# Kernel optimization log

Hardware: AMD Instinct MI355X
Metric: run time of the kernel (lower is better)

Reference implementation:

```python
import jax, jax.numpy as jnp
import numpy as np

DIM = 768
HID = 3072
E_SPEC = 4
E_SHARED = 2
TOP_K = 2
LN_EPS = 1e-5


def _expert_stack_params(key, n_experts):
    k1, k2, k3, k4 = jax.random.split(key, 4)
    s1 = 1.0 / np.sqrt(DIM)
    s2 = 1.0 / np.sqrt(HID)
    return {
        'w1': jax.random.uniform(k1, (n_experts, DIM, HID), minval=-s1, maxval=s1, dtype=jnp.float32),
        'b1': jax.random.uniform(k2, (n_experts, HID), minval=-s1, maxval=s1, dtype=jnp.float32),
        'w2': jax.random.uniform(k3, (n_experts, HID, DIM), minval=-s2, maxval=s2, dtype=jnp.float32),
        'b2': jax.random.uniform(k4, (n_experts, DIM), minval=-s2, maxval=s2, dtype=jnp.float32),
    }


def setup_inputs() -> dict:
    key = jax.random.key(0)
    ks = jax.random.split(key, 8)
    B, N = 64, 196
    s = 1.0 / np.sqrt(DIM)
    spec = _expert_stack_params(ks[1], E_SPEC)
    shared = _expert_stack_params(ks[2], E_SHARED)
    return {
        'x': jax.random.normal(ks[0], (B, N, DIM), dtype=jnp.float32),
        'ln_gamma': jnp.ones((DIM,), jnp.float32),
        'ln_beta': jnp.zeros((DIM,), jnp.float32),
        'spec_router_w': jax.random.uniform(ks[3], (DIM, E_SPEC), minval=-s, maxval=s, dtype=jnp.float32),
        'spec_router_b': jnp.zeros((E_SPEC,), jnp.float32),
        'spec_w1': spec['w1'], 'spec_b1': spec['b1'], 'spec_w2': spec['w2'], 'spec_b2': spec['b2'],
        'shared_router_w': jax.random.uniform(ks[4], (DIM, E_SHARED), minval=-s, maxval=s, dtype=jnp.float32),
        'shared_router_b': jnp.zeros((E_SHARED,), jnp.float32),
        'sh_w1': shared['w1'], 'sh_b1': shared['b1'], 'sh_w2': shared['w2'], 'sh_b2': shared['b2'],
    }


def _all_experts(x, w1, b1, w2, b2):
    # x: [B,N,D]; w1: [E,D,H] -> out: [B,N,E,D]
    h = jnp.einsum('bnd,edh->bneh', x, w1) + b1
    h = jax.nn.gelu(h, approximate=False)  # torch nn.GELU default is exact
    return jnp.einsum('bneh,ehd->bned', h, w2) + b2


def reference(x, ln_gamma, ln_beta,
              spec_router_w, spec_router_b, spec_w1, spec_b1, spec_w2, spec_b2,
              shared_router_w, shared_router_b, sh_w1, sh_b1, sh_w2, sh_b2):
    # LayerNorm
    mu = jnp.mean(x, axis=-1, keepdims=True)
    var = jnp.mean(jnp.square(x - mu), axis=-1, keepdims=True)
    xn = (x - mu) * jax.lax.rsqrt(var + LN_EPS) * ln_gamma + ln_beta

    # Specific-expert branch: dense all-expert compute, then top-k gather (faithful)
    spec_logits = xn @ spec_router_w + spec_router_b            # [B,N,E]
    spec_probs = jax.nn.softmax(spec_logits, axis=-1)
    topk_probs, topk_idx = jax.lax.top_k(spec_probs, TOP_K)    # [B,N,K]
    spec_out_all = _all_experts(xn, spec_w1, spec_b1, spec_w2, spec_b2)  # [B,N,E,D]
    sel = jnp.take_along_axis(spec_out_all, topk_idx[..., None], axis=2)  # [B,N,K,D]
    specific_out = jnp.sum(topk_probs[..., None] * sel, axis=2)

    # Shared-expert branch: softmax-weighted sum over all experts
    sh_logits = xn @ shared_router_w + shared_router_b          # [B,N,Es]
    sh_probs = jax.nn.softmax(sh_logits, axis=-1)
    sh_out_all = _all_experts(xn, sh_w1, sh_b1, sh_w2, sh_b2)   # [B,N,Es,D]
    shared_out = jnp.einsum('bne,bned->bnd', sh_probs, sh_out_all)

    out = specific_out + shared_out
    return (out, spec_logits, spec_probs, topk_idx, topk_probs, sh_logits, sh_probs)
```

## Files before the change

kernel.cpp:

```cpp
#include <hip/hip_runtime.h>
#include <hip/hip_bf16.h>
#include <math.h>

#define NTOK 12544
#define DIM 768
#define HID 3072
#define NTILE_MAX 102
#define NSLOT_MAX (NTILE_MAX * 256)
#define NSDT 49
#define NVT (NTILE_MAX + 2 * NSDT)
#define NBKT 64
#define BKTCAP 256
#define LDSB 131072
#define LDSB1 49152

typedef __hip_bfloat16 bf16;
typedef __attribute__((ext_vector_type(8))) short short8v;
typedef __attribute__((ext_vector_type(4))) float f32x4;

#define GPTR(p)  ((const __attribute__((address_space(1))) void*)(p))
#define LDSPTR(p) ((__attribute__((address_space(3))) void*)(p))

__global__ __launch_bounds__(256) void conv_all_kernel(
    const float* __restrict__ spec_w1, const float* __restrict__ sh_w1,
    const float* __restrict__ spec_w2, const float* __restrict__ sh_w2,
    bf16* __restrict__ w1t, bf16* __restrict__ w2t,
    int* __restrict__ cnt2, int* __restrict__ slot_tok, float* __restrict__ slot_gate) {
    int z = blockIdx.y;
    int ti = blockIdx.x;
    int t = threadIdx.x;
    if (z == 0) {
        if (ti == 0) cnt2[t] = 0;
        if (ti < NTILE_MAX) {
            int s = ti * 256 + t;
            slot_tok[s] = 0; slot_gate[s] = 0.0f;
        }
    }
    const float* src; bf16* dst; int R, C, tr, tc;
    if (z < 6) {
        R = DIM; C = HID;
        src = (z < 4) ? spec_w1 + (size_t)z * R * C : sh_w1 + (size_t)(z - 4) * R * C;
        dst = w1t + (size_t)z * R * C;
        tr = ti % 12; tc = ti / 12;
    } else {
        int e = z - 6;
        R = HID; C = DIM;
        src = (e < 4) ? spec_w2 + (size_t)e * R * C : sh_w2 + (size_t)(e - 4) * R * C;
        dst = w2t + (size_t)e * R * C;
        tr = ti % 48; tc = ti / 48;
    }
    __shared__ float tile[64][65];
    int r0 = tr * 64, c0 = tc * 64;
    int lr = t >> 4, lc = (t & 15) * 4;
    #pragma unroll
    for (int ii = 0; ii < 4; ++ii) {
        float4 v = *(const float4*)&src[(size_t)(r0 + lr + 16 * ii) * C + c0 + lc];
        tile[lc + 0][lr + 16 * ii] = v.x;
        tile[lc + 1][lr + 16 * ii] = v.y;
        tile[lc + 2][lr + 16 * ii] = v.z;
        tile[lc + 3][lr + 16 * ii] = v.w;
    }
    __syncthreads();
    int oc = t >> 4, orr = (t & 15) * 4;
    #pragma unroll
    for (int ii = 0; ii < 4; ++ii) {
        union { ushort4 u4; bf16 h[4]; } pk;
        #pragma unroll
        for (int k = 0; k < 4; ++k)
            pk.h[k] = __float2bfloat16(tile[oc + 16 * ii][orr + k]);
        *(ushort4*)&dst[(size_t)(c0 + oc + 16 * ii) * R + r0 + orr] = pk.u4;
    }
}

__global__ void router_ln_kernel(const float* __restrict__ x,
                                 const float* __restrict__ lng, const float* __restrict__ lnb,
                                 const float* __restrict__ srw, const float* __restrict__ srb,
                                 const float* __restrict__ shw, const float* __restrict__ shb,
                                 bf16* __restrict__ xnb,
                                 float* __restrict__ spec_logits, float* __restrict__ spec_probs,
                                 float* __restrict__ topk_idx, float* __restrict__ topk_probs,
                                 float* __restrict__ sh_logits, float* __restrict__ sh_probs,
                                 float* __restrict__ gates,
                                 int* __restrict__ cnt2, int* __restrict__ tok2,
                                 float* __restrict__ gate2) {
    int t = blockIdx.x * 4 + (threadIdx.x >> 6);
    int bucket = blockIdx.x & (NBKT - 1);
    int lane = threadIdx.x & 63;
    const float* xr = x + (size_t)t * DIM;
    bf16* xb = xnb + (size_t)t * DIM;
    float v[12];
    float s = 0.0f;
    #pragma unroll
    for (int i = 0; i < 6; ++i) {
        float2 xv = *(const float2*)&xr[lane * 2 + 128 * i];
        v[2 * i] = xv.x; v[2 * i + 1] = xv.y;
        s += xv.x + xv.y;
    }
    #pragma unroll
    for (int o = 32; o > 0; o >>= 1) s += __shfl_xor(s, o, 64);
    float mean = s * (1.0f / 768.0f);
    float sq = 0.0f;
    #pragma unroll
    for (int i = 0; i < 12; ++i) { float d = v[i] - mean; sq += d * d; }
    #pragma unroll
    for (int o = 32; o > 0; o >>= 1) sq += __shfl_xor(sq, o, 64);
    float rstd = rsqrtf(sq * (1.0f / 768.0f) + 1e-5f);

    float acc[6] = {0, 0, 0, 0, 0, 0};
    #pragma unroll
    for (int i = 0; i < 6; ++i) {
        int d0 = lane * 2 + 128 * i;
        float xn0 = (v[2 * i]     - mean) * rstd * lng[d0]     + lnb[d0];
        float xn1 = (v[2 * i + 1] - mean) * rstd * lng[d0 + 1] + lnb[d0 + 1];
        union { unsigned u; bf16 h[2]; } pk;
        pk.h[0] = __float2bfloat16(xn0);
        pk.h[1] = __float2bfloat16(xn1);
        *(unsigned*)&xb[d0] = pk.u;
        float4 a = *(const float4*)&srw[d0 * 4];
        float4 b = *(const float4*)&srw[d0 * 4 + 4];
        acc[0] += xn0 * a.x + xn1 * b.x;
        acc[1] += xn0 * a.y + xn1 * b.y;
        acc[2] += xn0 * a.z + xn1 * b.z;
        acc[3] += xn0 * a.w + xn1 * b.w;
        float4 sw = *(const float4*)&shw[d0 * 2];
        acc[4] += xn0 * sw.x + xn1 * sw.z;
        acc[5] += xn0 * sw.y + xn1 * sw.w;
    }
    #pragma unroll
    for (int j = 0; j < 6; ++j) {
        #pragma unroll
        for (int o = 32; o > 0; o >>= 1) acc[j] += __shfl_xor(acc[j], o, 64);
    }
    if (lane == 0) {
        float l[4];
        #pragma unroll
        for (int j = 0; j < 4; ++j) l[j] = acc[j] + srb[j];
        float m = fmaxf(fmaxf(l[0], l[1]), fmaxf(l[2], l[3]));
        float e[4], ssum = 0.0f;
        #pragma unroll
        for (int j = 0; j < 4; ++j) { e[j] = expf(l[j] - m); ssum += e[j]; }
        float inv = 1.0f / ssum;
        float p[4];
        #pragma unroll
        for (int j = 0; j < 4; ++j) p[j] = e[j] * inv;
        int i0 = 0;
        for (int j = 1; j < 4; ++j) if (p[j] > p[i0]) i0 = j;
        int i1 = -1;
        for (int j = 0; j < 4; ++j) {
            if (j == i0) continue;
            if (i1 < 0 || p[j] > p[i1]) i1 = j;
        }
        float sl0 = acc[4] + shb[0], sl1 = acc[5] + shb[1];
        float sm = fmaxf(sl0, sl1);
        float se0 = expf(sl0 - sm), se1 = expf(sl1 - sm);
        float sinv = 1.0f / (se0 + se1);
        float sp0 = se0 * sinv, sp1 = se1 * sinv;

        #pragma unroll
        for (int j = 0; j < 4; ++j) {
            spec_logits[t * 4 + j] = l[j];
            spec_probs[t * 4 + j]  = p[j];
        }
        topk_idx[t * 2 + 0]   = (float)i0;
        topk_idx[t * 2 + 1]   = (float)i1;
        topk_probs[t * 2 + 0] = p[i0];
        topk_probs[t * 2 + 1] = p[i1];
        sh_logits[t * 2 + 0]  = sl0;
        sh_logits[t * 2 + 1]  = sl1;
        sh_probs[t * 2 + 0]   = sp0;
        sh_probs[t * 2 + 1]   = sp1;
        float gg[6] = {0, 0, 0, 0, sp0, sp1};
        gg[i0] = p[i0];
        gg[i1] = p[i1];
        #pragma unroll
        for (int j = 0; j < 6; ++j) gates[t * 6 + j] = gg[j];
        int c0 = i0 * NBKT + bucket;
        int pos0 = atomicAdd(&cnt2[c0], 1);
        tok2[c0 * BKTCAP + pos0]  = t * 2 + 0;
        gate2[c0 * BKTCAP + pos0] = p[i0];
        int c1 = i1 * NBKT + bucket;
        int pos1 = atomicAdd(&cnt2[c1], 1);
        tok2[c1 * BKTCAP + pos1]  = t * 2 + 1;
        gate2[c1 * BKTCAP + pos1] = p[i1];
    }
}

__global__ void plan_kernel(const int* __restrict__ cnt2, int* __restrict__ e_of_tile,
                            const int* __restrict__ tok2, const float* __restrict__ gate2,
                            int* __restrict__ slot_tok, float* __restrict__ slot_gate,
                            int* __restrict__ back) {
    __shared__ int sbase[4 * NBKT];
    __shared__ int offsE[5];
    __shared__ int etot[4];
    int tid = threadIdx.x, lane = tid & 63, wid = tid >> 6;
    int c = cnt2[wid * NBKT + lane];
    int inc = c;
    #pragma unroll
    for (int o = 1; o < 64; o <<= 1) {
        int tv = __shfl_up(inc, o, 64);
        if (lane >= o) inc += tv;
    }
    int exc = inc - c;
    if (lane == 63) etot[wid] = inc;
    __syncthreads();
    if (tid == 0) {
        int o = 0;
        for (int e = 0; e < 4; ++e) { offsE[e] = o; o += (etot[e] + 255) & ~255; }
        offsE[4] = o;
    }
    __syncthreads();
    sbase[tid] = offsE[wid] + exc;
    for (int idx = tid; idx < NTILE_MAX; idx += 256) {
        int s0 = idx * 256, e = -1;
        for (int j = 0; j < 4; ++j)
            if (s0 >= offsE[j] && s0 < offsE[j + 1]) e = j;
        e_of_tile[idx] = e;
    }
    __syncthreads();
    int bs = sbase[tid];
    int cc = cnt2[tid];
    for (int i = 0; i < cc; ++i) {
        int gs = bs + i;
        int tk = tok2[tid * BKTCAP + i];
        slot_tok[gs] = tk >> 1;
        slot_gate[gs] = gate2[tid * BKTCAP + i];
        back[tk] = gs;
    }
}

__global__ void gather_kernel(const bf16* __restrict__ xnb, const int* __restrict__ slot_tok,
                              bf16* __restrict__ xg) {
    int idx = blockIdx.x * 256 + threadIdx.x;
    int slot = idx / 96;
    int c = (idx % 96) * 8;
    int tok = slot_tok[slot];
    *(short8v*)&xg[(size_t)slot * DIM + c] = *(const short8v*)&xnb[(size_t)tok * DIM + c];
}

__device__ __forceinline__ int swz(int off) {
    return off ^ (((off >> 8) & 1) << 4) ^ (((off >> 9) & 1) << 5);
}

__device__ __forceinline__ void stage2(bf16* lds, int base_elems, int wid,
                                       const bf16* s0, const bf16* s1) {
    __builtin_amdgcn_global_load_lds(GPTR(s0), LDSPTR(lds + base_elems + wid * 512), 16, 0, 0);
    __builtin_amdgcn_global_load_lds(GPTR(s1), LDSPTR(lds + base_elems + 4096 + wid * 512), 16, 0, 0);
}

__device__ __forceinline__ void mfma16(const short8v a[4], const short8v b[4], f32x4 (*am)[4]) {
    #pragma unroll
    for (int i = 0; i < 4; ++i)
        #pragma unroll
        for (int j = 0; j < 4; ++j)
            am[i][j] = __builtin_amdgcn_mfma_f32_16x16x32_bf16(a[i], b[j], am[i][j], 0, 0, 0);
}

#define BARRIER() __builtin_amdgcn_s_barrier()
#define VMCNT4() asm volatile("s_waitcnt vmcnt(4)" ::: "memory")
#define VMCNT3() asm volatile("s_waitcnt vmcnt(3)" ::: "memory")
#define VMCNT0() asm volatile("s_waitcnt vmcnt(0)" ::: "memory")

__device__ __forceinline__ void read_a4(const bf16* lds, int buf, int ks, int wm, int mh,
                                        int lane, short8v a[4]) {
    const char* base = (const char*)lds + buf * 32768 + ks * 16384;
    #pragma unroll
    for (int i = 0; i < 4; ++i) {
        int off = (wm * 128 + mh * 64 + i * 16 + (lane & 15)) * 64 + ((lane >> 4) * 16);
        a[i] = *(const short8v*)(base + swz(off));
    }
}

__device__ __forceinline__ void read_b4(const bf16* lds, int buf, int ks, int wn,
                                        int lane, short8v b[4]) {
    const char* base = (const char*)lds + 65536 + buf * 32768 + ks * 16384;
    #pragma unroll
    for (int j = 0; j < 4; ++j) {
        int off = (wn * 64 + j * 16 + (lane & 15)) * 64 + ((lane >> 4) * 16);
        b[j] = *(const short8v*)(base + swz(off));
    }
}

template<int NT>
__device__ __forceinline__ void kloop8p(bf16* lds, const bf16* a0, const bf16* a1,
                                        const bf16* b0, const bf16* b1,
                                        int wm, int wn, int wid, int lane,
                                        f32x4 acc[8][4]) {
    stage2(lds, 0, wid, a0, a1);
    stage2(lds, 32768, wid, b0, b1);
    stage2(lds, 8192, wid, a0 + 32, a1 + 32);
    stage2(lds, 32768 + 8192, wid, b0 + 32, b1 + 32);
    VMCNT4();
    BARRIER();
    for (int t = 0; t < NT; ++t) {
        int buf = t & 1, nb = buf ^ 1;
        bool pre = (t + 1 < NT);
        short8v af[4], bfv[4];
        if (pre) stage2(lds, nb * 16384, wid, a0 + (t + 1) * 64, a1 + (t + 1) * 64);
        read_a4(lds, buf, 0, wm, 0, lane, af);
        read_b4(lds, buf, 0, wn, lane, bfv);
        BARRIER();
        __builtin_amdgcn_s_setprio(1);
        mfma16(af, bfv, &acc[0]);
        __builtin_amdgcn_s_setprio(0);
        BARRIER();
        if (pre) stage2(lds, 32768 + nb * 16384, wid, b0 + (t + 1) * 64, b1 + (t + 1) * 64);
        read_a4(lds, buf, 0, wm, 1, lane, af);
        BARRIER();
        __builtin_amdgcn_s_setprio(1);
        mfma16(af, bfv, &acc[4]);
        __builtin_amdgcn_s_setprio(0);
        if (pre) VMCNT4(); else VMCNT0();
        BARRIER();
        if (pre) stage2(lds, nb * 16384 + 8192, wid, a0 + (t + 1) * 64 + 32, a1 + (t + 1) * 64 + 32);
        read_a4(lds, buf, 1, wm, 0, lane, af);
        read_b4(lds, buf, 1, wn, lane, bfv);
        BARRIER();
        __builtin_amdgcn_s_setprio(1);
        mfma16(af, bfv, &acc[0]);
        __builtin_amdgcn_s_setprio(0);
        BARRIER();
        if (pre) stage2(lds, 32768 + nb * 16384 + 8192, wid, b0 + (t + 1) * 64 + 32, b1 + (t + 1) * 64 + 32);
        read_a4(lds, buf, 1, wm, 1, lane, af);
        BARRIER();
        __builtin_amdgcn_s_setprio(1);
        mfma16(af, bfv, &acc[4]);
        __builtin_amdgcn_s_setprio(0);
        if (pre) VMCNT4();
        BARRIER();
    }
}

__device__ __forceinline__ void read_a4_128(const bf16* lds, int cur, int wm,
                                            int lane, short8v a[4]) {
    const char* base = (const char*)lds + cur * 8192;
    #pragma unroll
    for (int i = 0; i < 4; ++i) {
        int off = (wm * 64 + i * 16 + (lane & 15)) * 64 + ((lane >> 4) * 16);
        a[i] = *(const short8v*)(base + swz(off));
    }
}

__device__ __forceinline__ void read_b4_128(const bf16* lds, int cur, int wn,
                                            int lane, short8v b[4]) {
    const char* base = (const char*)lds + 16384 + cur * 16384;
    #pragma unroll
    for (int j = 0; j < 4; ++j) {
        int off = (wn * 64 + j * 16 + (lane & 15)) * 64 + ((lane >> 4) * 16);
        b[j] = *(const short8v*)(base + swz(off));
    }
}

template<int NS>
__device__ __forceinline__ void kloop2p(bf16* lds, const bf16* aA,
                                        const bf16* b0, const bf16* b1,
                                        int wm, int wn, int wid, int lane,
                                        f32x4 acc[4][4]) {
    __builtin_amdgcn_global_load_lds(GPTR(aA), LDSPTR(lds + wid * 512), 16, 0, 0);
    stage2(lds, 8192, wid, b0, b1);
    for (int s = 0; s < NS; ++s) {
        int cur = s & 1, nb = cur ^ 1;
        bool pre = (s + 1 < NS);
        if (pre) {
            __builtin_amdgcn_global_load_lds(GPTR(aA + (s + 1) * 32),
                                             LDSPTR(lds + nb * 4096 + wid * 512), 16, 0, 0);
            stage2(lds, 8192 + nb * 8192, wid, b0 + (s + 1) * 32, b1 + (s + 1) * 32);
        }
        if (pre) VMCNT3(); else VMCNT0();
        BARRIER();
        short8v av[4], bv[4];
        read_a4_128(lds, cur, wm, lane, av);
        read_b4_128(lds, cur, wn, lane, bv);
        __builtin_amdgcn_s_setprio(1);
        mfma16(av, bv, &acc[0]);
        __builtin_amdgcn_s_setprio(0);
        BARRIER();
    }
}

__device__ __forceinline__ float gelu_exact(float v) {
    return 0.5f * v * (1.0f + erff(v * 0.70710678118654752f));
}

__device__ __forceinline__ float gelu_fast(float x) {
    float z = 0.70710678118654752f * x;
    float az = fabsf(z);
    float t = __builtin_amdgcn_rcpf(1.0f + 0.3275911f * az);
    float poly = t * (0.254829592f + t * (-0.284496736f + t * (1.421413741f +
                 t * (-1.453152027f + t * 1.061405429f))));
    float erfv = 1.0f - poly * __expf(-az * az);
    erfv = (z < 0.0f) ? -erfv : erfv;
    return 0.5f * x * (1.0f + erfv);
}

__global__ __launch_bounds__(512, 4) void gemm1_2p(
    const bf16* __restrict__ xg, const bf16* __restrict__ xnb,
    const bf16* __restrict__ w1t,
    const float* __restrict__ spec_b1, const float* __restrict__ sh_b1,
    const int* __restrict__ e_of_tile,
    bf16* __restrict__ Hbuf, int y_base) {
    extern __shared__ bf16 lds[];
    int bx = blockIdx.x, by = blockIdx.y;
    int lt = by >> 1, half = by & 1;
    int y = y_base + lt;
    int tid = threadIdx.x, wid = tid >> 6, lane = tid & 63;
    int wm = wid >> 2, wn = wid & 3;
    int PA = tid;
    int LA = PA ^ ((PA >> 4) & 1) ^ (((PA >> 5) & 1) << 1);
    int ra = LA >> 2, ca = (LA & 3) * 8;
    int P0c = tid, P1c = 512 + tid;
    int L0 = P0c ^ ((P0c >> 4) & 1) ^ (((P0c >> 5) & 1) << 1);
    int L1 = P1c ^ ((P1c >> 4) & 1) ^ (((P1c >> 5) & 1) << 1);
    int rb0 = L0 >> 2, cb0 = (L0 & 3) * 8;
    int rb1 = L1 >> 2, cb1 = (L1 & 3) * 8;

    const bf16 *abase, *Bw;
    const float* bias;
    if (y < NTILE_MAX) {
        int e = e_of_tile[y];
        if (e < 0) return;
        abase = xg + (size_t)(y * 256 + half * 128) * DIM;
        Bw = w1t + (size_t)e * HID * DIM;
        bias = spec_b1 + (size_t)e * HID;
    } else {
        int ys = y - NTILE_MAX;
        int z = ys / NSDT, ry = ys % NSDT;
        abase = xnb + (size_t)(ry * 256 + half * 128) * DIM;
        Bw = w1t + (size_t)(4 + z) * HID * DIM;
        bias = sh_b1 + (size_t)z * HID;
    }
    const bf16* aA = abase + (size_t)ra * DIM + ca;
    const bf16* b0 = Bw + (size_t)(bx * 256 + rb0) * DIM + cb0;
    const bf16* b1 = Bw + (size_t)(bx * 256 + rb1) * DIM + cb1;

    f32x4 acc[4][4] = {};
    kloop2p<DIM / 32>(lds, aA, b0, b1, wm, wn, wid, lane, acc);

    bf16* hb = Hbuf + (size_t)(lt * 256 + half * 128) * HID;
    int fr = lane & 15, fq = lane >> 4;
    int cb = bx * 256 + wn * 64;
    #pragma unroll
    for (int j = 0; j < 4; ++j) {
        int col = cb + j * 16 + fr;
        float bv = bias[col];
        #pragma unroll
        for (int i = 0; i < 4; ++i) {
            #pragma unroll
            for (int rr = 0; rr < 4; ++rr) {
                int row = wm * 64 + i * 16 + fq * 4 + rr;
                hb[(size_t)row * HID + col] = __float2bfloat16(gelu_fast(acc[i][j][rr] + bv));
            }
        }
    }
}

__global__ __launch_bounds__(512, 2) void gemm2_8p(
    const bf16* __restrict__ Hbuf, const bf16* __restrict__ w2t,
    const float* __restrict__ spec_b2, const float* __restrict__ sh_b2,
    const int* __restrict__ e_of_tile, const float* __restrict__ slot_gate,
    const float* __restrict__ sh_probs,
    bf16* __restrict__ spec_g, bf16* __restrict__ shg, int y_base) {
    extern __shared__ bf16 lds[];
    int bx = blockIdx.x, by = blockIdx.y;
    int y = by + y_base;
    int tid = threadIdx.x, wid = tid >> 6, lane = tid & 63;
    int wm = wid >> 2, wn = wid & 3;
    int P0c = tid, P1c = 512 + tid;
    int L0 = P0c ^ ((P0c >> 4) & 1) ^ (((P0c >> 5) & 1) << 1);
    int L1 = P1c ^ ((P1c >> 4) & 1) ^ (((P1c >> 5) & 1) << 1);
    int r0 = L0 >> 2, c0 = (L0 & 3) * 8;
    int r1 = L1 >> 2, c1 = (L1 & 3) * 8;

    const bf16 *Bw;
    const float* bias;
    bf16* obase;
    bool grouped = (y < NTILE_MAX);
    int z = 0, ry = 0;
    if (grouped) {
        int e = e_of_tile[y];
        if (e < 0) return;
        Bw = w2t + (size_t)e * DIM * HID;
        bias = spec_b2 + (size_t)e * DIM;
        obase = spec_g + (size_t)y * 256 * DIM;
    } else {
        int ys = y - NTILE_MAX;
        z = ys / NSDT; ry = ys % NSDT;
        Bw = w2t + (size_t)(4 + z) * DIM * HID;
        bias = sh_b2 + (size_t)z * DIM;
        obase = shg + (size_t)(z * NTOK + ry * 256) * DIM;
    }
    const bf16* Ah = Hbuf + (size_t)by * 256 * HID;
    const bf16* a0 = Ah + (size_t)r0 * HID + c0;
    const bf16* a1 = Ah + (size_t)r1 * HID + c1;
    const bf16* b0 = Bw + (size_t)(bx * 256 + r0) * HID + c0;
    const bf16* b1 = Bw + (size_t)(bx * 256 + r1) * HID + c1;

    f32x4 acc[8][4] = {};
    kloop8p<HID / 64>(lds, a0, a1, b0, b1, wm, wn, wid, lane, acc);

    int fr = lane & 15, fq = lane >> 4;
    int cb = bx * 256 + wn * 64;
    #pragma unroll
    for (int j = 0; j < 4; ++j) {
        int col = cb + j * 16 + fr;
        float bv = bias[col];
        #pragma unroll
        for (int ii = 0; ii < 8; ++ii) {
            #pragma unroll
            for (int rr = 0; rr < 4; ++rr) {
                int row = wm * 128 + (ii >> 2) * 64 + (ii & 3) * 16 + fq * 4 + rr;
                float g = grouped ? slot_gate[y * 256 + row]
                                  : sh_probs[(size_t)(ry * 256 + row) * 2 + z];
                obase[(size_t)row * DIM + col] = __float2bfloat16(g * (acc[ii][j][rr] + bv));
            }
        }
    }
}

__device__ __forceinline__ void stage_tile(const bf16* __restrict__ g, int ldg,
                                           bf16* lds, int tid) {
    int wave = tid >> 6, lane = tid & 63;
    #pragma unroll
    for (int q = 0; q < 2; ++q) {
        int chunk = wave * 2 + q;
        int row = chunk * 16 + (lane >> 2);
        int col = (lane & 3) * 8;
        __builtin_amdgcn_global_load_lds(GPTR(g + (size_t)row * ldg + col),
                                         LDSPTR(lds + chunk * 512), 16, 0, 0);
    }
}

__device__ __forceinline__ void mfma_step(const bf16* As, const bf16* Bs,
                                          int wr, int wc, int fr, int fq, f32x4 acc[4][4]) {
    short8v a[4], b[4];
    #pragma unroll
    for (int i = 0; i < 4; ++i) {
        a[i] = *(const short8v*)&As[(wr * 64 + i * 16 + fr) * 32 + fq * 8];
        b[i] = *(const short8v*)&Bs[(wc * 64 + i * 16 + fr) * 32 + fq * 8];
    }
    #pragma unroll
    for (int i = 0; i < 4; ++i)
        #pragma unroll
        for (int j = 0; j < 4; ++j)
            acc[i][j] = __builtin_amdgcn_mfma_f32_16x16x32_bf16(a[i], b[j], acc[i][j], 0, 0, 0);
}

__global__ __launch_bounds__(256) void gemm1_dense(
    const bf16* __restrict__ A, const bf16* __restrict__ BT,
    const float* __restrict__ bias, bf16* __restrict__ H) {
    __shared__ bf16 As[128 * 32];
    __shared__ bf16 Bs[128 * 32];
    int tid = threadIdx.x;
    int wid = tid >> 6, lane = tid & 63;
    int wr = wid >> 1, wc = wid & 1;
    int fr = lane & 15, fq = lane >> 4;
    const bf16* Ag = A + (size_t)(blockIdx.y * 128) * DIM;
    const bf16* Bg = BT + (size_t)(blockIdx.x * 128) * DIM;
    f32x4 acc[4][4] = {};
    for (int k0 = 0; k0 < DIM; k0 += 32) {
        stage_tile(Ag + k0, DIM, As, tid);
        stage_tile(Bg + k0, DIM, Bs, tid);
        __syncthreads();
        mfma_step(As, Bs, wr, wc, fr, fq, acc);
        __syncthreads();
    }
    int rbase = blockIdx.y * 128 + wr * 64;
    int cbase = blockIdx.x * 128 + wc * 64;
    #pragma unroll
    for (int j = 0; j < 4; ++j) {
        int col = cbase + j * 16 + fr;
        float bv = bias[col];
        #pragma unroll
        for (int i = 0; i < 4; ++i)
            #pragma unroll
            for (int r = 0; r < 4; ++r) {
                int row = rbase + i * 16 + fq * 4 + r;
                H[(size_t)row * HID + col] = __float2bfloat16(gelu_exact(acc[i][j][r] + bv));
            }
    }
}

__global__ __launch_bounds__(256) void gemm2_dense_out(
    const bf16* __restrict__ A, const bf16* __restrict__ BT,
    const float* __restrict__ bias, const float* __restrict__ gates,
    float* __restrict__ out, int gidx, int accum) {
    __shared__ bf16 As[128 * 32];
    __shared__ bf16 Bs[128 * 32];
    int tid = threadIdx.x;
    int wid = tid >> 6, lane = tid & 63;
    int wr = wid >> 1, wc = wid & 1;
    int fr = lane & 15, fq = lane >> 4;
    const bf16* Ag = A + (size_t)(blockIdx.y * 128) * HID;
    const bf16* Bg = BT + (size_t)(blockIdx.x * 128) * HID;
    f32x4 acc[4][4] = {};
    for (int k0 = 0; k0 < HID; k0 += 32) {
        stage_tile(Ag + k0, HID, As, tid);
        stage_tile(Bg + k0, HID, Bs, tid);
        __syncthreads();
        mfma_step(As, Bs, wr, wc, fr, fq, acc);
        __syncthreads();
    }
    int rbase = blockIdx.y * 128 + wr * 64;
    int cbase = blockIdx.x * 128 + wc * 64;
    #pragma unroll
    for (int j = 0; j < 4; ++j) {
        int col = cbase + j * 16 + fr;
        float bv = bias[col];
        #pragma unroll
        for (int i = 0; i < 4; ++i)
            #pragma unroll
            for (int r = 0; r < 4; ++r) {
                int row = rbase + i * 16 + fq * 4 + r;
                float g = gates[(size_t)row * 6 + gidx];
                float v = g * (acc[i][j][r] + bv);
                size_t idx = (size_t)row * DIM + col;
                out[idx] = accum ? out[idx] + v : v;
            }
    }
}

__global__ void combine_kernel(const bf16* __restrict__ spec_g, const bf16* __restrict__ shg,
                               const int* __restrict__ back, float* __restrict__ out) {
    int idx = blockIdx.x * 256 + threadIdx.x;
    int tok = idx / 96;
    int c = (idx % 96) * 8;
    int b0 = back[2 * tok], b1 = back[2 * tok + 1];
    short8v q0 = *(const short8v*)&spec_g[(size_t)b0 * DIM + c];
    short8v q1 = *(const short8v*)&spec_g[(size_t)b1 * DIM + c];
    short8v s0 = *(const short8v*)&shg[(size_t)tok * DIM + c];
    short8v s1 = *(const short8v*)&shg[(size_t)(NTOK + tok) * DIM + c];
    float o[8];
    #pragma unroll
    for (int k = 0; k < 8; ++k) {
        float f0 = __uint_as_float((unsigned)(unsigned short)q0[k] << 16);
        float f1 = __uint_as_float((unsigned)(unsigned short)q1[k] << 16);
        float f2 = __uint_as_float((unsigned)(unsigned short)s0[k] << 16);
        float f3 = __uint_as_float((unsigned)(unsigned short)s1[k] << 16);
        o[k] = f0 + f1 + f2 + f3;
    }
    float* op = out + (size_t)tok * DIM + c;
    *(float4*)(op)     = *(const float4*)(o);
    *(float4*)(op + 4) = *(const float4*)(o + 4);
}

static inline size_t align256(size_t x) { return (x + 255) & ~(size_t)255; }

extern "C" void kernel_launch(void* const* d_in, const int* in_sizes, int n_in,
                              void* d_out, int out_size, void* d_ws, size_t ws_size,
                              hipStream_t stream) {
    const float* x      = (const float*)d_in[0];
    const float* gamma  = (const float*)d_in[1];
    const float* beta   = (const float*)d_in[2];
    const float* srw    = (const float*)d_in[3];
    const float* srb    = (const float*)d_in[4];
    const float* spec_w1 = (const float*)d_in[5];
    const float* spec_b1 = (const float*)d_in[6];
    const float* spec_w2 = (const float*)d_in[7];
    const float* spec_b2 = (const float*)d_in[8];
    const float* shw    = (const float*)d_in[9];
    const float* shb    = (const float*)d_in[10];
    const float* sh_w1  = (const float*)d_in[11];
    const float* sh_b1  = (const float*)d_in[12];
    const float* sh_w2  = (const float*)d_in[13];
    const float* sh_b2  = (const float*)d_in[14];

    char* p = (char*)d_ws;
    size_t off = 0;
    bf16* xnb = (bf16*)(p + off);       off = align256(off + (size_t)NTOK * DIM * 2);
    bf16* w1t = (bf16*)(p + off);       off = align256(off + (size_t)6 * HID * DIM * 2);
    bf16* w2t = (bf16*)(p + off);       off = align256(off + (size_t)6 * DIM * HID * 2);
    int*  cnt2 = (int*)(p + off);       off = align256(off + (size_t)4 * NBKT * 4);
    float* gates = (float*)(p + off);   off = align256(off + (size_t)NTOK * 6 * 4);
    int*  tok2 = (int*)(p + off);       off = align256(off + (size_t)4 * NBKT * BKTCAP * 4);
    float* gate2 = (float*)(p + off);   off = align256(off + (size_t)4 * NBKT * BKTCAP * 4);
    int*  slot_tok = (int*)(p + off);   off = align256(off + (size_t)NSLOT_MAX * 4);
    float* slot_gate = (float*)(p + off); off = align256(off + (size_t)NSLOT_MAX * 4);
    int*  back = (int*)(p + off);       off = align256(off + (size_t)2 * NTOK * 4);
    int*  e_of_tile = (int*)(p + off);  off = align256(off + (size_t)NTILE_MAX * 4);
    bf16* spec_g = (bf16*)(p + off);    off = align256(off + (size_t)NSLOT_MAX * DIM * 2);
    bf16* shg   = (bf16*)(p + off);     off = align256(off + (size_t)2 * NTOK * DIM * 2);
    size_t fixed_end = off;
    bf16* Hbuf = (bf16*)(p + fixed_end);
    bf16* xg = spec_g;

    const size_t tile_bytes = (size_t)256 * HID * 2;
    size_t avail = (ws_size > fixed_end) ? (ws_size - fixed_end) : 0;
    int tcap = (int)(avail / tile_bytes);
    if (tcap > NVT) tcap = NVT;

    float* out         = (float*)d_out;
    float* spec_logits = out + (size_t)NTOK * DIM;
    float* spec_probs  = spec_logits + (size_t)NTOK * 4;
    float* topk_idx    = spec_probs  + (size_t)NTOK * 4;
    float* topk_probs  = topk_idx    + (size_t)NTOK * 2;
    float* sh_logits   = topk_probs  + (size_t)NTOK * 2;
    float* sh_probs    = sh_logits   + (size_t)NTOK * 2;

    conv_all_kernel<<<dim3(576, 12), 256, 0, stream>>>(
        spec_w1, sh_w1, spec_w2, sh_w2, w1t, w2t, cnt2, slot_tok, slot_gate);

    router_ln_kernel<<<NTOK / 4, 256, 0, stream>>>(x, gamma, beta, srw, srb, shw, shb, xnb,
                                                   spec_logits, spec_probs, topk_idx,
                                                   topk_probs, sh_logits, sh_probs, gates,
                                                   cnt2, tok2, gate2);

    if (tcap >= 8) {
        plan_kernel<<<1, 256, 0, stream>>>(cnt2, e_of_tile, tok2, gate2,
                                           slot_tok, slot_gate, back);
        gather_kernel<<<NSLOT_MAX * 96 / 256, 256, 0, stream>>>(xnb, slot_tok, xg);
        int csz = tcap >= 67 ? (NVT + 2) / 3 : (tcap < 64 ? tcap : 64);
        if (csz > tcap) csz = tcap;
        for (int c0 = 0; c0 < NVT; c0 += csz) {
            int n = NVT - c0 < csz ? NVT - c0 : csz;
            gemm1_2p<<<dim3(HID / 256, 2 * n), 512, LDSB1, stream>>>(
                xg, xnb, w1t, spec_b1, sh_b1, e_of_tile, Hbuf, c0);
            gemm2_8p<<<dim3(DIM / 256, n), 512, LDSB, stream>>>(
                Hbuf, w2t, spec_b2, sh_b2, e_of_tile, slot_gate, sh_probs,
                spec_g, shg, c0);
        }
        combine_kernel<<<NTOK * 96 / 256, 256, 0, stream>>>(spec_g, shg, back, out);
    } else {
        bf16* HB = spec_g;
        for (int e = 0; e < 6; ++e) {
            const bf16* w1p = w1t + (size_t)e * HID * DIM;
            const bf16* w2p = w2t + (size_t)e * DIM * HID;
            const float* b1p = (e < 4) ? spec_b1 + (size_t)e * HID : sh_b1 + (size_t)(e - 4) * HID;
            const float* b2p = (e < 4) ? spec_b2 + (size_t)e * DIM : sh_b2 + (size_t)(e - 4) * DIM;
            gemm1_dense<<<dim3(HID / 128, NTOK / 128), 256, 0, stream>>>(xnb, w1p, b1p, HB);
            gemm2_dense_out<<<dim3(DIM / 128, NTOK / 128), 256, 0, stream>>>(
                HB, w2p, b2p, gates, out, e, e > 0);
        }
    }
}
```

Baseline: 839.6 us.

## Fuse weight conversion with LayerNorm/router and split gemm2 into half-row tiles

Merges the weight transpose/convert kernel and the LayerNorm/router kernel into one launch, with the counter reset moved to a memset, so both phases can overlap on the GPU. Rewrites gemm2 to handle 128-row halves with the smaller LDS footprint and the kloop2p pipeline shared with gemm1. Launch bounds now allow 4 blocks per CU, doubling the grid to raise occupancy. Smaller tiles cost more weight reloads per output row and may change the MFMA/LDS balance.

```diff
diff --git a/kernel.cpp b/kernel.cpp
--- a/kernel.cpp
+++ b/kernel.cpp
@@ -11,8 +11,8 @@
 #define NVT (NTILE_MAX + 2 * NSDT)
 #define NBKT 64
 #define BKTCAP 256
-#define LDSB 131072
 #define LDSB1 49152
+#define NCONVB 6912
 
 typedef __hip_bfloat16 bf16;
 typedef __attribute__((ext_vector_type(8))) short short8v;
@@ -21,73 +21,71 @@
 #define GPTR(p)  ((const __attribute__((address_space(1))) void*)(p))
 #define LDSPTR(p) ((__attribute__((address_space(3))) void*)(p))
 
-__global__ __launch_bounds__(256) void conv_all_kernel(
+__global__ __launch_bounds__(256) void prep_kernel(
     const float* __restrict__ spec_w1, const float* __restrict__ sh_w1,
     const float* __restrict__ spec_w2, const float* __restrict__ sh_w2,
     bf16* __restrict__ w1t, bf16* __restrict__ w2t,
-    int* __restrict__ cnt2, int* __restrict__ slot_tok, float* __restrict__ slot_gate) {
-    int z = blockIdx.y;
-    int ti = blockIdx.x;
+    int* __restrict__ slot_tok, float* __restrict__ slot_gate,
+    const float* __restrict__ x,
+    const float* __restrict__ lng, const float* __restrict__ lnb,
+    const float* __restrict__ srw, const float* __restrict__ srb,
+    const float* __restrict__ shw, const float* __restrict__ shb,
+    bf16* __restrict__ xnb,
+    float* __restrict__ spec_logits, float* __restrict__ spec_probs,
+    float* __restrict__ topk_idx, float* __restrict__ topk_probs,
+    float* __restrict__ sh_logits, float* __restrict__ sh_probs,
+    float* __restrict__ gates,
+    int* __restrict__ cnt2, int* __restrict__ tok2, float* __restrict__ gate2) {
+    __shared__ float tile[64][65];
+    int bid = blockIdx.x;
     int t = threadIdx.x;
-    if (z == 0) {
-        if (ti == 0) cnt2[t] = 0;
-        if (ti < NTILE_MAX) {
+    if (bid < NCONVB) {
+        int z = bid / 576, ti = bid % 576;
+        if (z == 0 && ti < NTILE_MAX) {
             int s = ti * 256 + t;
             slot_tok[s] = 0; slot_gate[s] = 0.0f;
         }
-    }
-    const float* src; bf16* dst; int R, C, tr, tc;
-    if (z < 6) {
-        R = DIM; C = HID;
-        src = (z < 4) ? spec_w1 + (size_t)z * R * C : sh_w1 + (size_t)(z - 4) * R * C;
-        dst = w1t + (size_t)z * R * C;
-        tr = ti % 12; tc = ti / 12;
-    } else {
-        int e = z - 6;
-        R = HID; C = DIM;
-        src = (e < 4) ? spec_w2 + (size_t)e * R * C : sh_w2 + (size_t)(e - 4) * R * C;
-        dst = w2t + (size_t)e * R * C;
-        tr = ti % 48; tc = ti / 48;
-    }
-    __shared__ float tile[64][65];
-    int r0 = tr * 64, c0 = tc * 64;
-    int lr = t >> 4, lc = (t & 15) * 4;
-    #pragma unroll
-    for (int ii = 0; ii < 4; ++ii) {
-        float4 v = *(const float4*)&src[(size_t)(r0 + lr + 16 * ii) * C + c0 + lc];
-        tile[lc + 0][lr + 16 * ii] = v.x;
-        tile[lc + 1][lr + 16 * ii] = v.y;
-        tile[lc + 2][lr + 16 * ii] = v.z;
-        tile[lc + 3][lr + 16 * ii] = v.w;
-    }
-    __syncthreads();
-    int oc = t >> 4, orr = (t & 15) * 4;
-    #pragma unroll
-    for (int ii = 0; ii < 4; ++ii) {
-        union { ushort4 u4; bf16 h[4]; } pk;
-        #pragma unroll
-        for (int k = 0; k < 4; ++k)
-            pk.h[k] = __float2bfloat16(tile[oc + 16 * ii][orr + k]);
-        *(ushort4*)&dst[(size_t)(c0 + oc + 16 * ii) * R + r0 + orr] = pk.u4;
-    }
-}
-
-__global__ void router_ln_kernel(const float* __restrict__ x,
-                                 const float* __restrict__ lng, const float* __restrict__ lnb,
-                                 const float* __restrict__ srw, const float* __restrict__ srb,
-                                 const float* __restrict__ shw, const float* __restrict__ shb,
-                                 bf16* __restrict__ xnb,
-                                 float* __restrict__ spec_logits, float* __restrict__ spec_probs,
-                                 float* __restrict__ topk_idx, float* __restrict__ topk_probs,
-                                 float* __restrict__ sh_logits, float* __restrict__ sh_probs,
-                                 float* __restrict__ gates,
-                                 int* __restrict__ cnt2, int* __restrict__ tok2,
-                                 float* __restrict__ gate2) {
-    int t = blockIdx.x * 4 + (threadIdx.x >> 6);
-    int bucket = blockIdx.x & (NBKT - 1);
-    int lane = threadIdx.x & 63;
-    const float* xr = x + (size_t)t * DIM;
-    bf16* xb = xnb + (size_t)t * DIM;
+        const float* src; bf16* dst; int R, C, tr, tc;
+        if (z < 6) {
+            R = DIM; C = HID;
+            src = (z < 4) ? spec_w1 + (size_t)z * R * C : sh_w1 + (size_t)(z - 4) * R * C;
+            dst = w1t + (size_t)z * R * C;
+            tr = ti % 12; tc = ti / 12;
+        } else {
+            int e = z - 6;
+            R = HID; C = DIM;
+            src = (e < 4) ? spec_w2 + (size_t)e * R * C : sh_w2 + (size_t)(e - 4) * R * C;
+            dst = w2t + (size_t)e * R * C;
+            tr = ti % 48; tc = ti / 48;
+        }
+        int r0 = tr * 64, c0 = tc * 64;
+        int lr = t >> 4, lc = (t & 15) * 4;
+        #pragma unroll
+        for (int ii = 0; ii < 4; ++ii) {
+            float4 v = *(const float4*)&src[(size_t)(r0 + lr + 16 * ii) * C + c0 + lc];
+            tile[lc + 0][lr + 16 * ii] = v.x;
+            tile[lc + 1][lr + 16 * ii] = v.y;
+            tile[lc + 2][lr + 16 * ii] = v.z;
+            tile[lc + 3][lr + 16 * ii] = v.w;
+        }
+        __syncthreads();
+        int oc = t >> 4, orr = (t & 15) * 4;
+        #pragma unroll
+        for (int ii = 0; ii < 4; ++ii) {
+            union { ushort4 u4; bf16 h[4]; } pk;
+            #pragma unroll
+            for (int k = 0; k < 4; ++k)
+                pk.h[k] = __float2bfloat16(tile[oc + 16 * ii][orr + k]);
+            *(ushort4*)&dst[(size_t)(c0 + oc + 16 * ii) * R + r0 + orr] = pk.u4;
+        }
+        return;
+    }
+    int rid = bid - NCONVB;
+    int tok = rid * 4 + (t >> 6);
+    int bucket = rid & (NBKT - 1);
+    int lane = t & 63;
+    const float* xr = x + (size_t)tok * DIM;
+    bf16* xb = xnb + (size_t)tok * DIM;
     float v[12];
     float s = 0.0f;
     #pragma unroll
@@ -158,29 +156,29 @@
 
         #pragma unroll
         for (int j = 0; j < 4; ++j) {
-            spec_logits[t * 4 + j] = l[j];
-            spec_probs[t * 4 + j]  = p[j];
-        }
-        topk_idx[t * 2 + 0]   = (float)i0;
-        topk_idx[t * 2 + 1]   = (float)i1;
-        topk_probs[t * 2 + 0] = p[i0];
-        topk_probs[t * 2 + 1] = p[i1];
-        sh_logits[t * 2 + 0]  = sl0;
-        sh_logits[t * 2 + 1]  = sl1;
-        sh_probs[t * 2 + 0]   = sp0;
-        sh_probs[t * 2 + 1]   = sp1;
+            spec_logits[tok * 4 + j] = l[j];
+            spec_probs[tok * 4 + j]  = p[j];
+        }
+        topk_idx[tok * 2 + 0]   = (float)i0;
+        topk_idx[tok * 2 + 1]   = (float)i1;
+        topk_probs[tok * 2 + 0] = p[i0];
+        topk_probs[tok * 2 + 1] = p[i1];
+        sh_logits[tok * 2 + 0]  = sl0;
+        sh_logits[tok * 2 + 1]  = sl1;
+        sh_probs[tok * 2 + 0]   = sp0;
+        sh_probs[tok * 2 + 1]   = sp1;
         float gg[6] = {0, 0, 0, 0, sp0, sp1};
         gg[i0] = p[i0];
         gg[i1] = p[i1];
         #pragma unroll
-        for (int j = 0; j < 6; ++j) gates[t * 6 + j] = gg[j];
+        for (int j = 0; j < 6; ++j) gates[tok * 6 + j] = gg[j];
         int c0 = i0 * NBKT + bucket;
         int pos0 = atomicAdd(&cnt2[c0], 1);
-        tok2[c0 * BKTCAP + pos0]  = t * 2 + 0;
+        tok2[c0 * BKTCAP + pos0]  = tok * 2 + 0;
         gate2[c0 * BKTCAP + pos0] = p[i0];
         int c1 = i1 * NBKT + bucket;
         int pos1 = atomicAdd(&cnt2[c1], 1);
-        tok2[c1 * BKTCAP + pos1]  = t * 2 + 1;
+        tok2[c1 * BKTCAP + pos1]  = tok * 2 + 1;
         gate2[c1 * BKTCAP + pos1] = p[i1];
     }
 }
@@ -256,79 +254,8 @@
 }
 
 #define BARRIER() __builtin_amdgcn_s_barrier()
-#define VMCNT4() asm volatile("s_waitcnt vmcnt(4)" ::: "memory")
 #define VMCNT3() asm volatile("s_waitcnt vmcnt(3)" ::: "memory")
 #define VMCNT0() asm volatile("s_waitcnt vmcnt(0)" ::: "memory")
-
-__device__ __forceinline__ void read_a4(const bf16* lds, int buf, int ks, int wm, int mh,
-                                        int lane, short8v a[4]) {
-    const char* base = (const char*)lds + buf * 32768 + ks * 16384;
-    #pragma unroll
-    for (int i = 0; i < 4; ++i) {
-        int off = (wm * 128 + mh * 64 + i * 16 + (lane & 15)) * 64 + ((lane >> 4) * 16);
-        a[i] = *(const short8v*)(base + swz(off));
-    }
-}
-
-__device__ __forceinline__ void read_b4(const bf16* lds, int buf, int ks, int wn,
-                                        int lane, short8v b[4]) {
-    const char* base = (const char*)lds + 65536 + buf * 32768 + ks * 16384;
-    #pragma unroll
-    for (int j = 0; j < 4; ++j) {
-        int off = (wn * 64 + j * 16 + (lane & 15)) * 64 + ((lane >> 4) * 16);
-        b[j] = *(const short8v*)(base + swz(off));
-    }
-}
-
-template<int NT>
-__device__ __forceinline__ void kloop8p(bf16* lds, const bf16* a0, const bf16* a1,
-                                        const bf16* b0, const bf16* b1,
-                                        int wm, int wn, int wid, int lane,
-                                        f32x4 acc[8][4]) {
-    stage2(lds, 0, wid, a0, a1);
-    stage2(lds, 32768, wid, b0, b1);
-    stage2(lds, 8192, wid, a0 + 32, a1 + 32);
-    stage2(lds, 32768 + 8192, wid, b0 + 32, b1 + 32);
-    VMCNT4();
-    BARRIER();
-    for (int t = 0; t < NT; ++t) {
-        int buf = t & 1, nb = buf ^ 1;
-        bool pre = (t + 1 < NT);
-        short8v af[4], bfv[4];
-        if (pre) stage2(lds, nb * 16384, wid, a0 + (t + 1) * 64, a1 + (t + 1) * 64);
-        read_a4(lds, buf, 0, wm, 0, lane, af);
-        read_b4(lds, buf, 0, wn, lane, bfv);
-        BARRIER();
-        __builtin_amdgcn_s_setprio(1);
-        mfma16(af, bfv, &acc[0]);
-        __builtin_amdgcn_s_setprio(0);
-        BARRIER();
-        if (pre) stage2(lds, 32768 + nb * 16384, wid, b0 + (t + 1) * 64, b1 + (t + 1) * 64);
-        read_a4(lds, buf, 0, wm, 1, lane, af);
-        BARRIER();
-        __builtin_amdgcn_s_setprio(1);
-        mfma16(af, bfv, &acc[4]);
-        __builtin_amdgcn_s_setprio(0);
-        if (pre) VMCNT4(); else VMCNT0();
-        BARRIER();
-        if (pre) stage2(lds, nb * 16384 + 8192, wid, a0 + (t + 1) * 64 + 32, a1 + (t + 1) * 64 + 32);
-        read_a4(lds, buf, 1, wm, 0, lane, af);
-        read_b4(lds, buf, 1, wn, lane, bfv);
-        BARRIER();
-        __builtin_amdgcn_s_setprio(1);
-        mfma16(af, bfv, &acc[0]);
-        __builtin_amdgcn_s_setprio(0);
-        BARRIER();
-        if (pre) stage2(lds, 32768 + nb * 16384 + 8192, wid, b0 + (t + 1) * 64 + 32, b1 + (t + 1) * 64 + 32);
-        read_a4(lds, buf, 1, wm, 1, lane, af);
-        BARRIER();
-        __builtin_amdgcn_s_setprio(1);
-        mfma16(af, bfv, &acc[4]);
-        __builtin_amdgcn_s_setprio(0);
-        if (pre) VMCNT4();
-        BARRIER();
-    }
-}
 
 __device__ __forceinline__ void read_a4_128(const bf16* lds, int cur, int wm,
                                             int lane, short8v a[4]) {
@@ -453,7 +380,7 @@
     }
 }
 
-__global__ __launch_bounds__(512, 2) void gemm2_8p(
+__global__ __launch_bounds__(512, 4) void gemm2_2p(
     const bf16* __restrict__ Hbuf, const bf16* __restrict__ w2t,
     const float* __restrict__ spec_b2, const float* __restrict__ sh_b2,
     const int* __restrict__ e_of_tile, const float* __restrict__ slot_gate,
@@ -461,16 +388,20 @@
     bf16* __restrict__ spec_g, bf16* __restrict__ shg, int y_base) {
     extern __shared__ bf16 lds[];
     int bx = blockIdx.x, by = blockIdx.y;
-    int y = by + y_base;
+    int lt = by >> 1, half = by & 1;
+    int y = y_base + lt;
     int tid = threadIdx.x, wid = tid >> 6, lane = tid & 63;
     int wm = wid >> 2, wn = wid & 3;
+    int PA = tid;
+    int LA = PA ^ ((PA >> 4) & 1) ^ (((PA >> 5) & 1) << 1);
+    int ra = LA >> 2, ca = (LA & 3) * 8;
     int P0c = tid, P1c = 512 + tid;
     int L0 = P0c ^ ((P0c >> 4) & 1) ^ (((P0c >> 5) & 1) << 1);
     int L1 = P1c ^ ((P1c >> 4) & 1) ^ (((P1c >> 5) & 1) << 1);
-    int r0 = L0 >> 2, c0 = (L0 & 3) * 8;
-    int r1 = L1 >> 2, c1 = (L1 & 3) * 8;
-
-    const bf16 *Bw;
+    int rb0 = L0 >> 2, cb0 = (L0 & 3) * 8;
+    int rb1 = L1 >> 2, cb1 = (L1 & 3) * 8;
+
+    const bf16* Bw;
     const float* bias;
     bf16* obase;
     bool grouped = (y < NTILE_MAX);
@@ -480,37 +411,37 @@
         if (e < 0) return;
         Bw = w2t + (size_t)e * DIM * HID;
         bias = spec_b2 + (size_t)e * DIM;
-        obase = spec_g + (size_t)y * 256 * DIM;
+        obase = spec_g + (size_t)(y * 256 + half * 128) * DIM;
     } else {
         int ys = y - NTILE_MAX;
         z = ys / NSDT; ry = ys % NSDT;
         Bw = w2t + (size_t)(4 + z) * DIM * HID;
         bias = sh_b2 + (size_t)z * DIM;
-        obase = shg + (size_t)(z * NTOK + ry * 256) * DIM;
-    }
-    const bf16* Ah = Hbuf + (size_t)by * 256 * HID;
-    const bf16* a0 = Ah + (size_t)r0 * HID + c0;
-    const bf16* a1 = Ah + (size_t)r1 * HID + c1;
-    const bf16* b0 = Bw + (size_t)(bx * 256 + r0) * HID + c0;
-    const bf16* b1 = Bw + (size_t)(bx * 256 + r1) * HID + c1;
-
-    f32x4 acc[8][4] = {};
-    kloop8p<HID / 64>(lds, a0, a1, b0, b1, wm, wn, wid, lane, acc);
+        obase = shg + (size_t)(z * NTOK + ry * 256 + half * 128) * DIM;
+    }
+    const bf16* Ah = Hbuf + (size_t)(lt * 256 + half * 128) * HID;
+    const bf16* aA = Ah + (size_t)ra * HID + ca;
+    const bf16* b0 = Bw + (size_t)(bx * 256 + rb0) * HID + cb0;
+    const bf16* b1 = Bw + (size_t)(bx * 256 + rb1) * HID + cb1;
+
+    f32x4 acc[4][4] = {};
+    kloop2p<HID / 32>(lds, aA, b0, b1, wm, wn, wid, lane, acc);
 
     int fr = lane & 15, fq = lane >> 4;
     int cb = bx * 256 + wn * 64;
+    int rowbase = half * 128;
     #pragma unroll
     for (int j = 0; j < 4; ++j) {
         int col = cb + j * 16 + fr;
         float bv = bias[col];
         #pragma unroll
-        for (int ii = 0; ii < 8; ++ii) {
+        for (int i = 0; i < 4; ++i) {
             #pragma unroll
             for (int rr = 0; rr < 4; ++rr) {
-                int row = wm * 128 + (ii >> 2) * 64 + (ii & 3) * 16 + fq * 4 + rr;
-                float g = grouped ? slot_gate[y * 256 + row]
-                                  : sh_probs[(size_t)(ry * 256 + row) * 2 + z];
-                obase[(size_t)row * DIM + col] = __float2bfloat16(g * (acc[ii][j][rr] + bv));
+                int row = wm * 64 + i * 16 + fq * 4 + rr;
+                float g = grouped ? slot_gate[y * 256 + rowbase + row]
+                                  : sh_probs[(size_t)(ry * 256 + rowbase + row) * 2 + z];
+                obase[(size_t)row * DIM + col] = __float2bfloat16(g * (acc[i][j][rr] + bv));
             }
         }
     }
@@ -695,13 +626,12 @@
     float* sh_logits   = topk_probs  + (size_t)NTOK * 2;
     float* sh_probs    = sh_logits   + (size_t)NTOK * 2;
 
-    conv_all_kernel<<<dim3(576, 12), 256, 0, stream>>>(
-        spec_w1, sh_w1, spec_w2, sh_w2, w1t, w2t, cnt2, slot_tok, slot_gate);
-
-    router_ln_kernel<<<NTOK / 4, 256, 0, stream>>>(x, gamma, beta, srw, srb, shw, shb, xnb,
-                                                   spec_logits, spec_probs, topk_idx,
-                                                   topk_probs, sh_logits, sh_probs, gates,
-                                                   cnt2, tok2, gate2);
+    hipMemsetAsync(cnt2, 0, (size_t)4 * NBKT * 4, stream);
+    prep_kernel<<<NCONVB + NTOK / 4, 256, 0, stream>>>(
+        spec_w1, sh_w1, spec_w2, sh_w2, w1t, w2t, slot_tok, slot_gate,
+        x, gamma, beta, srw, srb, shw, shb, xnb,
+        spec_logits, spec_probs, topk_idx, topk_probs, sh_logits, sh_probs,
+        gates, cnt2, tok2, gate2);
 
     if (tcap >= 8) {
         plan_kernel<<<1, 256, 0, stream>>>(cnt2, e_of_tile, tok2, gate2,
@@ -713,7 +643,7 @@
             int n = NVT - c0 < csz ? NVT - c0 : csz;
             gemm1_2p<<<dim3(HID / 256, 2 * n), 512, LDSB1, stream>>>(
                 xg, xnb, w1t, spec_b1, sh_b1, e_of_tile, Hbuf, c0);
-            gemm2_8p<<<dim3(DIM / 256, n), 512, LDSB, stream>>>(
+            gemm2_2p<<<dim3(DIM / 256, 2 * n), 512, LDSB1, stream>>>(
                 Hbuf, w2t, spec_b2, sh_b2, e_of_tile, slot_gate, sh_probs,
                 spec_g, shg, c0);
         }
```

Result: no change. 851.0 us (+1.4%).
